# Kernel tuning notes

Hardware: AMD Instinct MI355X
Metric: run time of the kernel (lower is better)

## Reference

```python
import jax, jax.numpy as jnp
import numpy as np

LN_EPS = 1e-5

def _layer_norm(x, g, b):
    m = x.mean(axis=-1, keepdims=True)
    v = x.var(axis=-1, keepdims=True)
    return (x - m) * jax.lax.rsqrt(v + LN_EPS) * g + b

def setup_inputs() -> dict:
    key = jax.random.key(0)
    ks = jax.random.split(key, 8)
    B, T, Din, D = 4, 4096, 1024, 1024
    s = 0.02
    return {
        "x": jax.random.normal(ks[0], (B, T, Din), jnp.float32),
        "hidden": jnp.zeros((B, 1, D), jnp.float32),
        "rnn_start": jnp.zeros((B, T, 1), jnp.float32),
        # EnsembleLinear(input_dim, d_model, ensemble=2): [2, Din, D] weights
        "Win": jax.random.normal(ks[1], (2, Din, D), jnp.float32) * s,
        "bin_": jnp.zeros((2, D), jnp.float32),
        "Wout": jax.random.normal(ks[2], (D, D), jnp.float32) * s,
        "bout": jnp.zeros((D,), jnp.float32),
        "W1": jax.random.normal(ks[3], (D, D), jnp.float32) * s,
        "b1": jnp.zeros((D,), jnp.float32),
        "W2": jax.random.normal(ks[4], (D, D), jnp.float32) * s,
        "b2": jnp.zeros((D,), jnp.float32),
        "ln_g": jnp.ones((D,), jnp.float32),
        "ln_b": jnp.zeros((D,), jnp.float32),
    }

def reference(x, hidden, rnn_start, Win, bin_, Wout, bout, W1, b1, W2, b2, ln_g, ln_b):
    # in_proj (ensemble of 2 linears): u[0]=v, u[1]=f
    u = jnp.einsum('btd,edk->ebtk', x, Win) + bin_[:, None, None, :]
    v = jnp.tanh(u[0])                      # [B,T,D]
    f = jax.nn.sigmoid(u[1])                # [B,T,D]
    f = f * (1.0 - rnn_start)               # reset gate at episode starts
    # gated linear recurrence (tied input gate): h_t = f_t*h_{t-1} + (1-f_t)*v_t
    h0 = hidden[:, 0, :]                    # [B,D]
    def step(h, vf):
        vt, ft = vf
        h = ft * h + (1.0 - ft) * vt
        return h, h
    hT, hs = jax.lax.scan(step, h0, (jnp.swapaxes(v, 0, 1), jnp.swapaxes(f, 0, 1)))
    hs = jnp.swapaxes(hs, 0, 1)             # [B,T,D]
    out = hs @ Wout + bout
    # PositionWiseFeedForward (dropout=0, eval): LN(w2(gelu(w1(x))) + x)
    x_ = jax.nn.gelu(out @ W1 + b1, approximate=False)
    out = _layer_norm(x_ @ W2 + b2 + out, ln_g, ln_b)
    hidden_new = hT[None, :, :]             # [1,B,D] (transpose(0,1) of [B,1,D])
    return out, hidden_new
```

## Files before the change

kernel.cpp:

```cpp
#include <hip/hip_runtime.h>
#include <hip/hip_bf16.h>
#include <math.h>

typedef __hip_bfloat16 bf16;
typedef __bf16  bf16x8  __attribute__((ext_vector_type(8)));
typedef float   floatx4 __attribute__((ext_vector_type(4)));

typedef const __attribute__((address_space(1))) void global_cv_t;
typedef __attribute__((address_space(3))) void       lds_v_t;

static __device__ __forceinline__ float bf2f(bf16 h) { return __bfloat162float(h); }
static __device__ __forceinline__ bf16  f2bf(float f) { return __float2bfloat16(f); }

__device__ __forceinline__ void load_lds16(const void* g, void* l) {
    __builtin_amdgcn_global_load_lds((global_cv_t*)g, (lds_v_t*)l, 16, 0, 0);
}

__global__ __launch_bounds__(256) void convx_k(const float4* __restrict__ in,
                                               bf16* __restrict__ out)
{
    const int i = blockIdx.x * 256 + threadIdx.x;
    const float4 v = in[i];
    bf16* o = out + (size_t)i * 4;
    o[0] = f2bf(v.x); o[1] = f2bf(v.y); o[2] = f2bf(v.z); o[3] = f2bf(v.w);
}

__global__ __launch_bounds__(256) void trc_k(
    const float* __restrict__ w0, const float* __restrict__ w1,
    const float* __restrict__ w2, const float* __restrict__ w3,
    const float* __restrict__ w4, bf16* __restrict__ dst)
{
    const float* src;
    switch (blockIdx.z) {
        case 0: src = w0; break;
        case 1: src = w1; break;
        case 2: src = w2; break;
        case 3: src = w3; break;
        default: src = w4; break;
    }
    bf16* d = dst + ((size_t)blockIdx.z << 20);
    __shared__ float tile[32][33];
    const int tx = threadIdx.x & 31;
    const int ty = threadIdx.x >> 5;
    const int bx = blockIdx.x * 32, by = blockIdx.y * 32;
#pragma unroll
    for (int j = 0; j < 32; j += 8)
        tile[ty + j][tx] = src[(size_t)(by + ty + j) * 1024 + bx + tx];
    __syncthreads();
#pragma unroll
    for (int j = 0; j < 32; j += 8)
        d[(size_t)(bx + ty + j) * 1024 + by + tx] = f2bf(tile[tx][ty + j]);
}

__global__ __launch_bounds__(256, 4) void gemm_k(
    const bf16* __restrict__ A, const bf16* __restrict__ Bt,
    const float* __restrict__ bias, const float* __restrict__ auxf,
    const bf16* __restrict__ auxb, bf16* __restrict__ Db,
    bf16* __restrict__ Db2, float* __restrict__ Df, const int mode)
{
    __shared__ alignas(16) bf16 As[128 * 64];
    __shared__ alignas(16) bf16 Bs[128 * 64];

    const int tid  = threadIdx.x;
    const int wave = tid >> 6;
    const int lane = tid & 63;
    const int quad = lane >> 4;
    const int l16  = lane & 15;
    const int sw   = l16 & 7;
    const int wm   = wave & 1;
    const int wn   = wave >> 1;
    const int bm   = blockIdx.x * 128;

    int bn, emode;
    const bf16* Bte = Bt;
    const float* biase = bias;
    bf16* Dbe = Db;
    if (mode == 5) {
        const int mat = blockIdx.y >> 3;
        bn    = (blockIdx.y & 7) * 128;
        Bte   = Bt + ((size_t)mat << 20);
        biase = bias + (mat << 10);
        Dbe   = mat ? Db2 : Db;
        emode = mat ? 1 : 0;
    } else {
        bn = blockIdx.y * 128;
        emode = mode;
    }

    const int srow  = lane >> 3;
    const int skoff = (((lane & 7) ^ srow) << 3);

    const bf16* gA = A   + (size_t)(bm + wave * 32 + srow) * 1024 + skoff;
    const bf16* gB = Bte + (size_t)(bn + wave * 32 + srow) * 1024 + skoff;
    bf16* lA = &As[wave * 2048];
    bf16* lB = &Bs[wave * 2048];

    floatx4 acc[4][4];
#pragma unroll
    for (int i = 0; i < 4; ++i)
#pragma unroll
        for (int j = 0; j < 4; ++j)
            acc[i][j] = (floatx4){0.f, 0.f, 0.f, 0.f};

    for (int k0 = 0; k0 < 1024; k0 += 64) {
        __syncthreads();
#pragma unroll
        for (int c = 0; c < 4; ++c) {
            load_lds16(gA + (size_t)c * 8192 + k0, lA + c * 512);
            load_lds16(gB + (size_t)c * 8192 + k0, lB + c * 512);
        }
        __syncthreads();

#pragma unroll
        for (int kk = 0; kk < 2; ++kk) {
            bf16x8 af[4], bfr[4];
#pragma unroll
            for (int t = 0; t < 4; ++t) {
                const int g = ((kk * 4 + quad) ^ sw) << 3;
                af[t]  = *(const bf16x8*)&As[(wm * 64 + t * 16 + l16) * 64 + g];
                bfr[t] = *(const bf16x8*)&Bs[(wn * 64 + t * 16 + l16) * 64 + g];
            }
#pragma unroll
            for (int tm = 0; tm < 4; ++tm)
#pragma unroll
                for (int tn = 0; tn < 4; ++tn)
                    acc[tm][tn] = __builtin_amdgcn_mfma_f32_16x16x32_bf16(
                        af[tm], bfr[tn], acc[tm][tn], 0, 0, 0);
        }
    }

    float bv[4];
#pragma unroll
    for (int tn = 0; tn < 4; ++tn)
        bv[tn] = biase[bn + wn * 64 + tn * 16 + l16];

#pragma unroll
    for (int tm = 0; tm < 4; ++tm) {
#pragma unroll
        for (int r = 0; r < 4; ++r) {
            const int gm = bm + wm * 64 + tm * 16 + quad * 4 + r;
            const size_t rowoff = (size_t)gm << 10;
            float rowmul = 1.f;
            if (emode == 1) rowmul = 1.f - auxf[gm];
#pragma unroll
            for (int tn = 0; tn < 4; ++tn) {
                const int gn = bn + wn * 64 + tn * 16 + l16;
                float val = acc[tm][tn][r] + bv[tn];
                if (emode == 0)      val = tanhf(val);
                else if (emode == 1) val = rowmul / (1.f + expf(-val));
                else if (emode == 3) val = 0.5f * val * (1.f + erff(val * 0.70710678118654752f));
                if (emode == 4) {
                    val += bf2f(auxb[rowoff + gn]);
                    Df[rowoff + gn] = val;
                } else {
                    Dbe[rowoff + gn] = f2bf(val);
                }
            }
        }
    }
}

__global__ __launch_bounds__(256) void scan1_k(
    const bf16* __restrict__ v, const bf16* __restrict__ f,
    float* __restrict__ Ac, float* __restrict__ Bc)
{
    const int idx = blockIdx.x * 256 + threadIdx.x;
    const int ch = idx & 4095;
    const int c  = idx >> 12;
    const int b  = ch >> 10, d = ch & 1023;
    const size_t base = ((size_t)(b * 4096 + c * 64) << 10) + d;
    float a = 1.f, hb = 0.f;
#pragma unroll 8
    for (int i = 0; i < 64; ++i) {
        const size_t o = base + ((size_t)i << 10);
        const float ft = bf2f(f[o]);
        const float vt = bf2f(v[o]);
        hb = fmaf(ft, hb, (1.f - ft) * vt);
        a *= ft;
    }
    Ac[c * 4096 + ch] = a;
    Bc[c * 4096 + ch] = hb;
}

__global__ __launch_bounds__(256) void scanmid_k(
    const float* __restrict__ Ac, const float* __restrict__ Bc,
    const float* __restrict__ hidden, float* __restrict__ Hin)
{
    const int ch = blockIdx.x * 256 + threadIdx.x;
    float h = hidden[ch];
#pragma unroll 8
    for (int c = 0; c < 64; ++c) {
        Hin[c * 4096 + ch] = h;
        h = fmaf(Ac[c * 4096 + ch], h, Bc[c * 4096 + ch]);
    }
}

__global__ __launch_bounds__(256) void scan2_k(
    const bf16* __restrict__ v, const bf16* __restrict__ f,
    const float* __restrict__ Hin, bf16* __restrict__ hs,
    float* __restrict__ hT)
{
    const int idx = blockIdx.x * 256 + threadIdx.x;
    const int ch = idx & 4095;
    const int c  = idx >> 12;
    const int b  = ch >> 10, d = ch & 1023;
    const size_t base = ((size_t)(b * 4096 + c * 64) << 10) + d;
    float h = Hin[c * 4096 + ch];
#pragma unroll 8
    for (int i = 0; i < 64; ++i) {
        const size_t o = base + ((size_t)i << 10);
        const float ft = bf2f(f[o]);
        const float vt = bf2f(v[o]);
        h = fmaf(ft, h, (1.f - ft) * vt);
        hs[o] = f2bf(h);
    }
    if (c == 63) hT[ch] = h;
}

__global__ __launch_bounds__(256) void ln_k(
    float* __restrict__ s, const float* __restrict__ g,
    const float* __restrict__ b)
{
    const int row = blockIdx.x;
    const int tid = threadIdx.x;
    const size_t off = (size_t)row << 10;
    const float4 xv = ((const float4*)(s + off))[tid];
    float sum = xv.x + xv.y + xv.z + xv.w;
    float sq  = xv.x * xv.x + xv.y * xv.y + xv.z * xv.z + xv.w * xv.w;
#pragma unroll
    for (int o = 32; o > 0; o >>= 1) {
        sum += __shfl_down(sum, o, 64);
        sq  += __shfl_down(sq,  o, 64);
    }
    __shared__ float s1[4], s2[4];
    if ((tid & 63) == 0) { s1[tid >> 6] = sum; s2[tid >> 6] = sq; }
    __syncthreads();
    sum = s1[0] + s1[1] + s1[2] + s1[3];
    sq  = s2[0] + s2[1] + s2[2] + s2[3];
    const float mean = sum * (1.f / 1024.f);
    const float var  = sq * (1.f / 1024.f) - mean * mean;
    const float rstd = rsqrtf(var + 1e-5f);
    const float4 gv = ((const float4*)g)[tid];
    const float4 bv = ((const float4*)b)[tid];
    float4 y;
    y.x = (xv.x - mean) * rstd * gv.x + bv.x;
    y.y = (xv.y - mean) * rstd * gv.y + bv.y;
    y.z = (xv.z - mean) * rstd * gv.z + bv.z;
    y.w = (xv.w - mean) * rstd * gv.w + bv.w;
    ((float4*)(s + off))[tid] = y;
}

extern "C" void kernel_launch(void* const* d_in, const int* in_sizes, int n_in,
                              void* d_out, int out_size, void* d_ws, size_t ws_size,
                              hipStream_t stream)
{
    const float* x         = (const float*)d_in[0];
    const float* hidden    = (const float*)d_in[1];
    const float* rnn_start = (const float*)d_in[2];
    const float* Win       = (const float*)d_in[3];
    const float* bin_      = (const float*)d_in[4];
    const float* Wout      = (const float*)d_in[5];
    const float* bout      = (const float*)d_in[6];
    const float* W1        = (const float*)d_in[7];
    const float* b1        = (const float*)d_in[8];
    const float* W2        = (const float*)d_in[9];
    const float* b2        = (const float*)d_in[10];
    const float* ln_g      = (const float*)d_in[11];
    const float* ln_b      = (const float*)d_in[12];
    float* out = (float*)d_out;
    float* hT  = out + (1u << 24);

    char* p = (char*)d_ws;
    bf16* Wt    = (bf16*)p;                    p += 5ull * (1u << 20) * sizeof(bf16);
    bf16* slotA = (bf16*)p;                    p += (1ull << 24) * sizeof(bf16);
    bf16* slotB = (bf16*)p;                    p += (1ull << 24) * sizeof(bf16);
    bf16* slotC = (bf16*)p;                    p += (1ull << 24) * sizeof(bf16);
    float* Ac  = (float*)p;                    p += (1ull << 18) * sizeof(float);
    float* Bc  = (float*)p;                    p += (1ull << 18) * sizeof(float);
    float* Hin = (float*)p;                    p += (1ull << 18) * sizeof(float);

    bf16* WoutT = Wt + 2u * (1u << 20);
    bf16* W1T   = Wt + 3u * (1u << 20);
    bf16* W2T   = Wt + 4u * (1u << 20);

    convx_k<<<16384, 256, 0, stream>>>((const float4*)x, slotA);
    trc_k<<<dim3(32, 32, 5), 256, 0, stream>>>(Win, Win + (1u << 20), Wout, W1, W2, Wt);

    gemm_k<<<dim3(128, 16), 256, 0, stream>>>(slotA, Wt, bin_, rnn_start, nullptr,
                                              slotB, slotC, nullptr, 5);

    scan1_k<<<1024, 256, 0, stream>>>(slotB, slotC, Ac, Bc);
    scanmid_k<<<16, 256, 0, stream>>>(Ac, Bc, hidden, Hin);
    scan2_k<<<1024, 256, 0, stream>>>(slotB, slotC, Hin, slotA, hT);

    gemm_k<<<dim3(128, 8), 256, 0, stream>>>(slotA, WoutT, bout, nullptr, nullptr,
                                             slotB, nullptr, nullptr, 2);
    gemm_k<<<dim3(128, 8), 256, 0, stream>>>(slotB, W1T,   b1,   nullptr, nullptr,
                                             slotC, nullptr, nullptr, 3);
    gemm_k<<<dim3(128, 8), 256, 0, stream>>>(slotC, W2T,   b2,   nullptr, slotB,
                                             nullptr, nullptr, out, 4);

    ln_k<<<16384, 256, 0, stream>>>(out, ln_g, ln_b);
}
```

Before: 418.0 us.

## Pack GEMM A operand in MFMA fragment order and load directly from global

Activations feeding the GEMMs are now stored in a pre-tiled layout that matches the MFMA 16x32 fragment order. The x conversion, the scan output and the intermediate GEMM outputs all write this layout, so each wave can load its A fragments straight from global memory without staging them through LDS. With the LDS freed, the B tile doubles its K depth to 128, which halves the number of barrier-separated iterations. The trade-off is that A reads now go directly to global/L2 with no LDS sharing between waves, and the scan and epilogue stores become scattered.

```diff
diff --git a/kernel.cpp b/kernel.cpp
--- a/kernel.cpp
+++ b/kernel.cpp
@@ -16,13 +16,38 @@
     __builtin_amdgcn_global_load_lds((global_cv_t*)g, (lds_v_t*)l, 16, 0, 0);
 }
 
-__global__ __launch_bounds__(256) void convx_k(const float4* __restrict__ in,
+__device__ __forceinline__ size_t paddr(int m, int k) {
+    return ((size_t)(m >> 4) << 14) + ((size_t)(k >> 5) << 9)
+         + (((k >> 3) & 3) << 7) + ((m & 15) << 3) + (k & 7);
+}
+
+__global__ __launch_bounds__(256) void packx_k(const float* __restrict__ in,
                                                bf16* __restrict__ out)
 {
-    const int i = blockIdx.x * 256 + threadIdx.x;
-    const float4 v = in[i];
-    bf16* o = out + (size_t)i * 4;
-    o[0] = f2bf(v.x); o[1] = f2bf(v.y); o[2] = f2bf(v.z); o[3] = f2bf(v.w);
+    __shared__ float t[16][260];
+    const int mt  = blockIdx.x;
+    const int k0  = blockIdx.y << 8;
+    const int tid = threadIdx.x;
+    const float* src = in + ((size_t)mt << 14) + k0;
+#pragma unroll
+    for (int j = 0; j < 4; ++j) {
+        const int idx = j * 256 + tid;
+        const int r = idx >> 6, c4 = (idx & 63) << 2;
+        const float4 v = *(const float4*)(src + (size_t)r * 1024 + c4);
+        t[r][c4] = v.x; t[r][c4 + 1] = v.y; t[r][c4 + 2] = v.z; t[r][c4 + 3] = v.w;
+    }
+    __syncthreads();
+    bf16* dst = out + ((size_t)mt << 14) + ((size_t)(k0 >> 5) << 9);
+#pragma unroll
+    for (int j = 0; j < 2; ++j) {
+        const int g = j * 256 + tid;
+        const int r = g & 15, quad = (g >> 4) & 3, kb = g >> 6;
+        const float* s = &t[r][kb * 32 + quad * 8];
+        union { bf16x8 v; bf16 h[8]; } u;
+#pragma unroll
+        for (int e = 0; e < 8; ++e) u.h[e] = f2bf(s[e]);
+        *(bf16x8*)(dst + ((size_t)kb << 9) + ((quad * 16 + r) << 3)) = u.v;
+    }
 }
 
 __global__ __launch_bounds__(256) void trc_k(
@@ -58,8 +83,7 @@
     const bf16* __restrict__ auxb, bf16* __restrict__ Db,
     bf16* __restrict__ Db2, float* __restrict__ Df, const int mode)
 {
-    __shared__ alignas(16) bf16 As[128 * 64];
-    __shared__ alignas(16) bf16 Bs[128 * 64];
+    __shared__ alignas(16) bf16 Bs[128 * 128];
 
     const int tid  = threadIdx.x;
     const int wave = tid >> 6;
@@ -87,13 +111,16 @@
         emode = mode;
     }
 
-    const int srow  = lane >> 3;
-    const int skoff = (((lane & 7) ^ srow) << 3);
-
-    const bf16* gA = A   + (size_t)(bm + wave * 32 + srow) * 1024 + skoff;
-    const bf16* gB = Bte + (size_t)(bn + wave * 32 + srow) * 1024 + skoff;
-    bf16* lA = &As[wave * 2048];
-    bf16* lB = &Bs[wave * 2048];
+    const int brow = lane >> 4;
+    const int bgq  = lane & 15;
+    const bf16* gB_e = Bte + (size_t)(bn + wave * 32 + brow) * 1024 + ((bgq ^ brow) << 3);
+    const bf16* gB_o = Bte + (size_t)(bn + wave * 32 + brow) * 1024 + ((bgq ^ (4 + brow)) << 3);
+    bf16* lB = &Bs[(wave * 32) * 128];
+
+    const bf16* pA[4];
+#pragma unroll
+    for (int t = 0; t < 4; ++t)
+        pA[t] = A + (((size_t)(bm >> 4) + wm * 4 + t) << 14) + (lane << 3);
 
     floatx4 acc[4][4];
 #pragma unroll
@@ -102,24 +129,25 @@
         for (int j = 0; j < 4; ++j)
             acc[i][j] = (floatx4){0.f, 0.f, 0.f, 0.f};
 
-    for (int k0 = 0; k0 < 1024; k0 += 64) {
+    for (int k0 = 0; k0 < 1024; k0 += 128) {
         __syncthreads();
 #pragma unroll
-        for (int c = 0; c < 4; ++c) {
-            load_lds16(gA + (size_t)c * 8192 + k0, lA + c * 512);
-            load_lds16(gB + (size_t)c * 8192 + k0, lB + c * 512);
+        for (int c = 0; c < 8; c += 2) {
+            load_lds16(gB_e + ((size_t)c << 12) + k0, lB + (c << 9));
+            load_lds16(gB_o + ((size_t)(c + 1) << 12) + k0, lB + ((c + 1) << 9));
         }
         __syncthreads();
 
 #pragma unroll
-        for (int kk = 0; kk < 2; ++kk) {
+        for (int kk = 0; kk < 4; ++kk) {
             bf16x8 af[4], bfr[4];
 #pragma unroll
-            for (int t = 0; t < 4; ++t) {
-                const int g = ((kk * 4 + quad) ^ sw) << 3;
-                af[t]  = *(const bf16x8*)&As[(wm * 64 + t * 16 + l16) * 64 + g];
-                bfr[t] = *(const bf16x8*)&Bs[(wn * 64 + t * 16 + l16) * 64 + g];
-            }
+            for (int t = 0; t < 4; ++t)
+                af[t] = *(const bf16x8*)(pA[t] + ((size_t)k0 << 4) + (kk << 9));
+#pragma unroll
+            for (int t = 0; t < 4; ++t)
+                bfr[t] = *(const bf16x8*)&Bs[(size_t)(wn * 64 + t * 16 + l16) * 128
+                                             + ((((kk << 2) + quad) ^ sw) << 3)];
 #pragma unroll
             for (int tm = 0; tm < 4; ++tm)
 #pragma unroll
@@ -146,14 +174,20 @@
             for (int tn = 0; tn < 4; ++tn) {
                 const int gn = bn + wn * 64 + tn * 16 + l16;
                 float val = acc[tm][tn][r] + bv[tn];
-                if (emode == 0)      val = tanhf(val);
-                else if (emode == 1) val = rowmul / (1.f + expf(-val));
-                else if (emode == 3) val = 0.5f * val * (1.f + erff(val * 0.70710678118654752f));
-                if (emode == 4) {
-                    val += bf2f(auxb[rowoff + gn]);
+                if (emode == 0) {
+                    val = tanhf(val);
+                    Dbe[rowoff + gn] = f2bf(val);
+                } else if (emode == 1) {
+                    val = rowmul / (1.f + expf(-val));
+                    Dbe[rowoff + gn] = f2bf(val);
+                } else if (emode == 2) {
+                    Dbe[paddr(gm, gn)] = f2bf(val);
+                } else if (emode == 3) {
+                    val = 0.5f * val * (1.f + erff(val * 0.70710678118654752f));
+                    Dbe[paddr(gm, gn)] = f2bf(val);
+                } else {
+                    val += bf2f(auxb[paddr(gm, gn)]);
                     Df[rowoff + gn] = val;
-                } else {
-                    Dbe[rowoff + gn] = f2bf(val);
                 }
             }
         }
@@ -205,6 +239,8 @@
     const int c  = idx >> 12;
     const int b  = ch >> 10, d = ch & 1023;
     const size_t base = ((size_t)(b * 4096 + c * 64) << 10) + d;
+    const int m0 = b * 4096 + c * 64;
+    const size_t dpart = ((size_t)(d >> 5) << 9) + (((d >> 3) & 3) << 7) + (d & 7);
     float h = Hin[c * 4096 + ch];
 #pragma unroll 8
     for (int i = 0; i < 64; ++i) {
@@ -212,7 +248,8 @@
         const float ft = bf2f(f[o]);
         const float vt = bf2f(v[o]);
         h = fmaf(ft, h, (1.f - ft) * vt);
-        hs[o] = f2bf(h);
+        const int m = m0 + i;
+        hs[((size_t)(m >> 4) << 14) + dpart + ((m & 15) << 3)] = f2bf(h);
     }
     if (c == 63) hT[ch] = h;
 }
@@ -283,7 +320,7 @@
     bf16* W1T   = Wt + 3u * (1u << 20);
     bf16* W2T   = Wt + 4u * (1u << 20);
 
-    convx_k<<<16384, 256, 0, stream>>>((const float4*)x, slotA);
+    packx_k<<<dim3(1024, 4), 256, 0, stream>>>(x, slotA);
     trc_k<<<dim3(32, 32, 5), 256, 0, stream>>>(Win, Win + (1u << 20), Wout, W1, W2, Wt);
 
     gemm_k<<<dim3(128, 16), 256, 0, stream>>>(slotA, Wt, bin_, rnn_start, nullptr,
```

Result: slower. 490.7 us (+17.4%).
